# Performance work log

Hardware: AMD Instinct MI355X
Metric: run time of the kernel (lower is better)

## Reference

```python
import math
import jax, jax.numpy as jnp
import numpy as np

B = 256          # graphs per batch
N0 = 512         # nodes per graph
DEG = 16         # avg degree
E = B * N0 * DEG # total edges
F_IN = 160
H = 64
RATIO = 0.11
NUM_CLASSES = 2


def setup_inputs() -> dict:
    key = jax.random.key(0)
    ks = jax.random.split(key, 20)
    x = jax.random.normal(ks[0], (B * N0, F_IN), jnp.float32)
    # within-graph random edges: src/dst local in [0, N0) plus graph offset
    eg = E // B
    off = (jnp.arange(B, dtype=jnp.int32) * N0)[:, None]
    src = (jax.random.randint(ks[1], (B, eg), 0, N0, jnp.int32) + off).reshape(-1)
    dst = (jax.random.randint(ks[2], (B, eg), 0, N0, jnp.int32) + off).reshape(-1)
    edge_index = jnp.stack([src, dst], 0)
    s = lambda fan: 1.0 / np.sqrt(fan)
    inp = {
        'x': x,
        'edge_index': edge_index,
        'conv1_Wr': jax.random.normal(ks[3], (F_IN, H), jnp.float32) * s(F_IN),
        'conv1_Wl': jax.random.normal(ks[4], (F_IN, H), jnp.float32) * s(F_IN),
        'conv1_b': jnp.zeros((H,), jnp.float32),
        'convs_Wr': jax.random.normal(ks[5], (5, H, H), jnp.float32) * s(H),
        'convs_Wl': jax.random.normal(ks[6], (5, H, H), jnp.float32) * s(H),
        'convs_b': jnp.zeros((5, H), jnp.float32),
        'pools_Wr': jax.random.normal(ks[7], (2, H, 1), jnp.float32) * s(H),
        'pools_Wl': jax.random.normal(ks[8], (2, H, 1), jnp.float32) * s(H),
        'pools_b': jnp.zeros((2, 1), jnp.float32),
        'lin1_W': jax.random.normal(ks[9], (6 * H, H), jnp.float32) * s(6 * H),
        'lin1_b': jnp.zeros((H,), jnp.float32),
        'lin2_W': jax.random.normal(ks[10], (H, NUM_CLASSES), jnp.float32) * s(H),
        'lin2_b': jnp.zeros((NUM_CLASSES,), jnp.float32),
    }
    return inp


def _gconv(x, src, dst, emask, Wr, Wl, b, n_nodes):
    # PyG GraphConv(aggr='mean'): lin_rel(mean_{j->i} x_j) + lin_root(x)
    msg = x[src] * emask[:, None]                              # [E, F]
    agg = jax.ops.segment_sum(msg, dst, num_segments=n_nodes)  # [N, F]
    deg = jax.ops.segment_sum(emask, dst, num_segments=n_nodes)
    agg = agg / jnp.maximum(deg, 1.0)[:, None]
    return agg @ Wr + b + x @ Wl


def _sag_pool(x, src, dst, emask, Wr, Wl, b, n_per, k):
    n_nodes = B * n_per
    score = _gconv(x, src, dst, emask, Wr, Wl, b, n_nodes)[:, 0]   # [N]
    _, idx = jax.lax.top_k(score.reshape(B, n_per), k)             # [B, k]
    perm = (idx + (jnp.arange(B, dtype=jnp.int32) * n_per)[:, None]).reshape(-1)
    new_x = x[perm] * jnp.tanh(score[perm])[:, None]
    newpos = jnp.full((n_nodes,), -1, jnp.int32).at[perm].set(
        jnp.arange(B * k, dtype=jnp.int32))
    ns, nd = newpos[src], newpos[dst]
    valid = (ns >= 0) & (nd >= 0)
    new_emask = emask * valid.astype(emask.dtype)
    return new_x, jnp.where(valid, ns, 0), jnp.where(valid, nd, 0), new_emask


def _gmp(x, n_per):  # global_mean_pool with equal-size graphs
    return x.reshape(B, n_per, -1).mean(axis=1)


def reference(x, edge_index, conv1_Wr, conv1_Wl, conv1_b, convs_Wr, convs_Wl,
              convs_b, pools_Wr, pools_Wl, pools_b, lin1_W, lin1_b,
              lin2_W, lin2_b):
    src, dst = edge_index[0], edge_index[1]
    emask = jnp.ones(src.shape, x.dtype)
    n = N0
    x = jax.nn.relu(_gconv(x, src, dst, emask, conv1_Wr, conv1_Wl, conv1_b, B * n))
    xs = [_gmp(x, n)]
    for i in range(5):
        x = jax.nn.relu(_gconv(x, src, dst, emask, convs_Wr[i], convs_Wl[i],
                               convs_b[i], B * n))
        xs.append(_gmp(x, n))
        if i % 2 == 0 and i < 4:
            j = i // 2
            k = math.ceil(RATIO * n)
            x, src, dst, emask = _sag_pool(x, src, dst, emask, pools_Wr[j],
                                           pools_Wl[j], pools_b[j], n, k)
            n = k
    h = jnp.concatenate(xs, axis=-1)          # JumpingKnowledge('cat') -> [B, 6H]
    h = jax.nn.relu(h @ lin1_W + lin1_b)
    h = h @ lin2_W + lin2_b                   # dropout is identity in eval mode
    return jax.nn.log_softmax(h, axis=-1)
```

## Files before the change

kernel.cpp:

```cpp
#include <hip/hip_runtime.h>
#include <math.h>

namespace {
constexpr int NB   = 256;
constexpr int EPG  = 8192;
constexpr int ETOT = NB * EPG;
constexpr int FH   = 64;
constexpr int NN0  = NB * 512;
}

__device__ float g_feat[1][(size_t)NN0 * FH];
__device__ float g_xs[NB * 6 * FH];
__device__ int   g_esrc[2][ETOT];
__device__ int   g_edst[2][ETOT];
__device__ int   g_ecnt[2][NB];

__global__ __launch_bounds__(1024)
void front(const float* __restrict__ x,
           const int* __restrict__ esrc, const int* __restrict__ edst,
           const float* __restrict__ c1Wr, const float* __restrict__ c1Wl,
           const float* __restrict__ c1b,
           const float* __restrict__ cWr, const float* __restrict__ cWl,
           const float* __restrict__ cb,
           const float* __restrict__ pwr, const float* __restrict__ pwl,
           const float* __restrict__ pb)
{
  __shared__ float zlds[512 * 64];
  __shared__ unsigned short csrbuf[EPG];
  __shared__ __align__(16) unsigned long long u2[512];
  __shared__ float wpf[2048];
  __shared__ int scnt;
  unsigned int* hist  = reinterpret_cast<unsigned int*>(u2);
  unsigned int* start = hist + 512;
  float* __restrict__ xnew = g_feat[0];
  const int g = blockIdx.x, t = threadIdx.x;
  const int gbase = g * 512, ebase = g * EPG;
  const int lane = t & 63, w = t >> 6;
  const int ndbase = w * 32;

  auto stage_chunk = [&](int c, int p) {
    const int xb  = p ? 8192  : 0;
    const int wrO = p ? 18432 : 16384;
    const int wlO = p ? 22528 : 20480;
    #pragma unroll
    for (int i = 0; i < 2; ++i) {
      const int slot = t + i * 1024;
      const int r = slot >> 2, q = slot & 3;
      const float* gp = &x[(size_t)(gbase + r) * 160 + c * 16 + q * 4];
      float* lp = zlds + xb + (size_t)(i * 1024 + w * 64) * 4;
      __builtin_amdgcn_global_load_lds(
          (const __attribute__((address_space(1))) unsigned int*)gp,
          (__attribute__((address_space(3))) unsigned int*)lp, 16, 0, 0);
    }
    {
      const float* gp = &c1Wr[c * 1024 + t];
      float* lp = zlds + wrO + (size_t)(w * 64);
      __builtin_amdgcn_global_load_lds(
          (const __attribute__((address_space(1))) unsigned int*)gp,
          (__attribute__((address_space(3))) unsigned int*)lp, 4, 0, 0);
    }
    {
      const float* gp = &c1Wl[c * 1024 + t];
      float* lp = zlds + wlO + (size_t)(w * 64);
      __builtin_amdgcn_global_load_lds(
          (const __attribute__((address_space(1))) unsigned int*)gp,
          (__attribute__((address_space(3))) unsigned int*)lp, 4, 0, 0);
    }
  };

  if (t < 512) hist[t] = 0;
  if (t == 0) scnt = 0;
  __syncthreads();
  stage_chunk(0, 0);
  for (int e = t; e < EPG; e += 1024)
    atomicAdd(&hist[edst[ebase + e] - gbase], 1u);
  __syncthreads();
  {
    unsigned int* sA = reinterpret_cast<unsigned int*>(wpf);
    unsigned int* sB = sA + 512;
    if (t < 512) sA[t] = hist[t];
    __syncthreads();
    unsigned int *pa = sA, *pb = sB;
    for (int off = 1; off < 512; off <<= 1) {
      if (t < 512) {
        unsigned int v = pa[t];
        if (t >= off) v += pa[t - off];
        pb[t] = v;
      }
      __syncthreads();
      unsigned int* tmp = pa; pa = pb; pb = tmp;
    }
    if (t < 512) start[t] = pa[t] - hist[t];
    __syncthreads();
    unsigned int* cur = pb;
    if (t < 512) cur[t] = start[t];
    __syncthreads();
    for (int e = t; e < EPG; e += 1024) {
      const int sl = esrc[ebase + e] - gbase;
      const int dl = edst[ebase + e] - gbase;
      const unsigned int pos = atomicAdd(&cur[dl], 1u);
      csrbuf[pos] = (unsigned short)sl;
    }
  }
  __syncthreads();
  float zacc[32], xla[32];
  #pragma unroll
  for (int i = 0; i < 32; ++i) { zacc[i] = 0.f; xla[i] = 0.f; }
  #pragma unroll 1
  for (int c = 0; c < 10; ++c) {
    if (c < 9) stage_chunk(c + 1, (c + 1) & 1);
    const int p   = c & 1;
    const int xb  = p ? 8192  : 0;
    const int wrO = p ? 18432 : 16384;
    const int wlO = p ? 22528 : 20480;
    #pragma unroll 1
    for (int k4 = 0; k4 < 4; ++k4) {
      const int kb = k4 * 4;
      const float wr0 = zlds[wrO + (kb+0)*64 + lane], wr1 = zlds[wrO + (kb+1)*64 + lane],
                  wr2 = zlds[wrO + (kb+2)*64 + lane], wr3 = zlds[wrO + (kb+3)*64 + lane];
      const float wl0 = zlds[wlO + (kb+0)*64 + lane], wl1 = zlds[wlO + (kb+1)*64 + lane],
                  wl2 = zlds[wlO + (kb+2)*64 + lane], wl3 = zlds[wlO + (kb+3)*64 + lane];
      #pragma unroll
      for (int i = 0; i < 32; ++i) {
        const float4 xv = *reinterpret_cast<const float4*>(
            &zlds[xb + (ndbase + i) * 16 + kb]);
        float za = zacc[i], xa = xla[i];
        za = fmaf(xv.x, wr0, za); za = fmaf(xv.y, wr1, za);
        za = fmaf(xv.z, wr2, za); za = fmaf(xv.w, wr3, za);
        xa = fmaf(xv.x, wl0, xa); xa = fmaf(xv.y, wl1, xa);
        xa = fmaf(xv.z, wl2, xa); xa = fmaf(xv.w, wl3, xa);
        zacc[i] = za; xla[i] = xa;
      }
    }
    __syncthreads();
  }
  #pragma unroll
  for (int i = 0; i < 32; ++i)
    zlds[(ndbase + i) * 64 + lane] = zacc[i];
  __syncthreads();
  {
    const float bv = c1b[lane];
    float psum = 0.f;
    #pragma unroll 1
    for (int i = 0; i < 32; ++i) {
      const int nd = ndbase + i;
      const unsigned int s = start[nd], d = hist[nd];
      float a0 = 0.f, a1 = 0.f, a2 = 0.f, a3 = 0.f;
      unsigned int j = 0;
      for (; j + 4 <= d; j += 4) {
        const int i0 = csrbuf[s+j], i1 = csrbuf[s+j+1],
                  i2 = csrbuf[s+j+2], i3 = csrbuf[s+j+3];
        a0 += zlds[i0*64 + lane]; a1 += zlds[i1*64 + lane];
        a2 += zlds[i2*64 + lane]; a3 += zlds[i3*64 + lane];
      }
      for (; j < d; ++j) a0 += zlds[csrbuf[s+j]*64 + lane];
      float v = ((a0 + a1) + (a2 + a3)) / (float)(d > 0 ? d : 1) + xla[i] + bv;
      v = fmaxf(v, 0.f);
      zacc[i] = v;
      psum += v;
    }
    __syncthreads();
    #pragma unroll
    for (int i = 0; i < 32; ++i)
      zlds[(ndbase + i) * 64 + lane] = zacc[i];
    wpf[w * 64 + lane] = psum;
    __syncthreads();
    if (t < 64) {
      float s = 0.f;
      #pragma unroll
      for (int ww = 0; ww < 16; ++ww) s += wpf[ww*64 + t];
      g_xs[g*384 + 0 + t] = s * (1.f/512.f);
    }
  }
  #pragma unroll
  for (int i = 0; i < 32; ++i) { zacc[i] = 0.f; xla[i] = 0.f; }
  {
    float* w_r = wpf;
    float* w_l = wpf + 1024;
    #pragma unroll 1
    for (int c = 0; c < 4; ++c) {
      __syncthreads();
      w_r[t] = cWr[c * 1024 + t];
      w_l[t] = cWl[c * 1024 + t];
      __syncthreads();
      #pragma unroll 1
      for (int k4 = 0; k4 < 4; ++k4) {
        const int kb = k4 * 4;
        const float wr0 = w_r[(kb+0)*64 + lane], wr1 = w_r[(kb+1)*64 + lane],
                    wr2 = w_r[(kb+2)*64 + lane], wr3 = w_r[(kb+3)*64 + lane];
        const float wl0 = w_l[(kb+0)*64 + lane], wl1 = w_l[(kb+1)*64 + lane],
                    wl2 = w_l[(kb+2)*64 + lane], wl3 = w_l[(kb+3)*64 + lane];
        #pragma unroll
        for (int i = 0; i < 32; ++i) {
          const float4 xv = *reinterpret_cast<const float4*>(
              &zlds[(ndbase + i) * 64 + c * 16 + kb]);
          float za = zacc[i], xa = xla[i];
          za = fmaf(xv.x, wr0, za); za = fmaf(xv.y, wr1, za);
          za = fmaf(xv.z, wr2, za); za = fmaf(xv.w, wr3, za);
          xa = fmaf(xv.x, wl0, xa); xa = fmaf(xv.y, wl1, xa);
          xa = fmaf(xv.z, wl2, xa); xa = fmaf(xv.w, wl3, xa);
          zacc[i] = za; xla[i] = xa;
        }
      }
    }
  }
  __syncthreads();
  #pragma unroll
  for (int i = 0; i < 32; ++i)
    zlds[(ndbase + i) * 64 + lane] = zacc[i];
  __syncthreads();
  {
    const float bv = cb[lane];
    float psum = 0.f;
    #pragma unroll 1
    for (int i = 0; i < 32; ++i) {
      const int nd = ndbase + i;
      const unsigned int s = start[nd], d = hist[nd];
      float a0 = 0.f, a1 = 0.f, a2 = 0.f, a3 = 0.f;
      unsigned int j = 0;
      for (; j + 4 <= d; j += 4) {
        const int i0 = csrbuf[s+j], i1 = csrbuf[s+j+1],
                  i2 = csrbuf[s+j+2], i3 = csrbuf[s+j+3];
        a0 += zlds[i0*64 + lane]; a1 += zlds[i1*64 + lane];
        a2 += zlds[i2*64 + lane]; a3 += zlds[i3*64 + lane];
      }
      for (; j < d; ++j) a0 += zlds[csrbuf[s+j]*64 + lane];
      float v = ((a0 + a1) + (a2 + a3)) / (float)(d > 0 ? d : 1) + xla[i] + bv;
      v = fmaxf(v, 0.f);
      zacc[i] = v;
      psum += v;
    }
    __syncthreads();
    #pragma unroll
    for (int i = 0; i < 32; ++i)
      zlds[(ndbase + i) * 64 + lane] = zacc[i];
    wpf[w * 64 + lane] = psum;
    __syncthreads();
    if (t < 64) {
      float s = 0.f;
      #pragma unroll
      for (int ww = 0; ww < 16; ++ww) s += wpf[ww*64 + t];
      g_xs[g*384 + 64 + t] = s * (1.f/512.f);
    }
    __syncthreads();
  }
  float* zs     = wpf;
  float* swl    = wpf + 512;
  float* sscore = wpf + 1024;
  const float pwrv = pwr[lane], pwlv = pwl[lane];
  for (int nd = w; nd < 512; nd += 16) {
    const float v = zlds[nd*64 + lane];
    float a = v * pwrv, b = v * pwlv;
    #pragma unroll
    for (int off = 32; off > 0; off >>= 1) {
      a += __shfl_xor(a, off);
      b += __shfl_xor(b, off);
    }
    if (lane == 0) { zs[nd] = a; swl[nd] = b; }
  }
  __syncthreads();
  if (t < 512) {
    const unsigned int s = start[t], d = hist[t];
    float a = 0.f;
    for (unsigned int j = 0; j < d; ++j) a += zs[csrbuf[s + j]];
    sscore[t] = a / fmaxf((float)d, 1.f) + pb[0] + swl[t];
  }
  __syncthreads();
  unsigned long long* keys = u2;
  if (t < 512) {
    unsigned int u = __float_as_uint(sscore[t]);
    u = (u & 0x80000000u) ? ~u : (u | 0x80000000u);
    keys[t] = ((unsigned long long)u << 32) | (unsigned int)(~(unsigned int)t);
  }
  __syncthreads();
  for (int kk = 2; kk <= 512; kk <<= 1) {
    for (int j = kk >> 1; j > 0; j >>= 1) {
      if (t < 512) {
        const int ixj = t ^ j;
        if (ixj > t) {
          const unsigned long long a = keys[t], bk = keys[ixj];
          const bool up = ((t & kk) == 0);
          if (up ? (a < bk) : (a > bk)) { keys[t] = bk; keys[ixj] = a; }
        }
      }
      __syncthreads();
    }
  }
  short* np = reinterpret_cast<short*>(csrbuf);
  if (t < 512) np[t] = -1;
  __syncthreads();
  if (t < 57)
    np[(int)(~(unsigned int)(keys[t] & 0xffffffffull))] = (short)t;
  __syncthreads();
  for (int r = w; r < 57; r += 16) {
    const int old = (int)(~(unsigned int)(keys[r] & 0xffffffffull));
    const float sc = tanhf(sscore[old]);
    xnew[(size_t)(g*57 + r)*64 + lane] = zlds[old*64 + lane] * sc;
  }
  for (int e = t; e < EPG; e += 1024) {
    const int sl = esrc[ebase + e] - gbase;
    const int dl = edst[ebase + e] - gbase;
    const int ns = np[sl], nd2 = np[dl];
    if (ns >= 0 && nd2 >= 0) {
      const int slot = atomicAdd(&scnt, 1);
      g_esrc[0][ebase + slot] = g*57 + ns;
      g_edst[0][ebase + slot] = g*57 + nd2;
    }
  }
  __syncthreads();
  if (t == 0) g_ecnt[0][g] = scnt;
}

__device__ __forceinline__ void conv_small(
    float* X, float* Z, float* ACC, float* w_s, const float* deg,
    const float* Wr, const float* Wl, const float* bias,
    int n, const int* esrc, const int* edst, int m, int gb, int ebase,
    int xs_off, int g, int t, int lane, int w)
{
  for (int i = t; i < n*64; i += 512) { Z[i] = 0.f; ACC[i] = 0.f; }
  __syncthreads();
  for (int kc = 0; kc < 4; ++kc) {
    for (int i = t; i < 1024; i += 512) w_s[i] = Wr[kc*1024 + i];
    __syncthreads();
    for (int r = w; r < n; r += 8) {
      float zacc = 0.f;
      #pragma unroll
      for (int k = 0; k < 16; ++k)
        zacc = fmaf(X[r*64 + kc*16 + k], w_s[k*64 + lane], zacc);
      Z[r*64 + lane] += zacc;
    }
    __syncthreads();
  }
  for (int e = w; e < m; e += 8) {
    const int sl = esrc[ebase + e] - gb;
    const int dl = edst[ebase + e] - gb;
    atomicAdd(&ACC[dl*64 + lane], Z[sl*64 + lane]);
  }
  __syncthreads();
  for (int i = t; i < n*64; i += 512) {
    const int r = i >> 6, f = i & 63;
    Z[i] = ACC[i] / fmaxf(deg[r], 1.f) + bias[f];
  }
  __syncthreads();
  for (int kc = 0; kc < 4; ++kc) {
    for (int i = t; i < 1024; i += 512) w_s[i] = Wl[kc*1024 + i];
    __syncthreads();
    for (int r = w; r < n; r += 8) {
      float zacc = 0.f;
      #pragma unroll
      for (int k = 0; k < 16; ++k)
        zacc = fmaf(X[r*64 + kc*16 + k], w_s[k*64 + lane], zacc);
      Z[r*64 + lane] += zacc;
    }
    __syncthreads();
  }
  for (int i = t; i < n*64; i += 512) X[i] = fmaxf(Z[i], 0.f);
  __syncthreads();
  if (t < 64) {
    float s = 0.f;
    for (int r = 0; r < n; ++r) s += X[r*64 + t];
    g_xs[g*384 + xs_off + t] = s / (float)n;
  }
  __syncthreads();
}

__global__ __launch_bounds__(512)
void tail(const float* __restrict__ cWr, const float* __restrict__ cWl,
          const float* __restrict__ cb,
          const float* __restrict__ pWr, const float* __restrict__ pWl,
          const float* __restrict__ pb)
{
  __shared__ float X[57*64], Z[57*64], ACC[57*64];
  __shared__ float w_s[16*64];
  __shared__ float deg[64];
  __shared__ float zs[64], swl[64], sagg[64], sscore[64];
  __shared__ unsigned long long keys[64];
  __shared__ short newpos[64];
  __shared__ int scnt;
  const int g = blockIdx.x, t = threadIdx.x;
  const int lane = t & 63, w = t >> 6;
  const int ebase = g * EPG;

  for (int i = t; i < 57*64; i += 512) X[i] = g_feat[0][(size_t)(g*57)*64 + i];
  const int m0 = g_ecnt[0][g];
  if (t < 64) deg[t] = 0.f;
  __syncthreads();
  for (int e = t; e < m0; e += 512)
    atomicAdd(&deg[g_edst[0][ebase + e] - g*57], 1.f);
  __syncthreads();

  conv_small(X, Z, ACC, w_s, deg, cWr + 4096,  cWl + 4096,  cb + 64,
             57, g_esrc[0], g_edst[0], m0, g*57, ebase, 128, g, t, lane, w);
  conv_small(X, Z, ACC, w_s, deg, cWr + 8192,  cWl + 8192,  cb + 128,
             57, g_esrc[0], g_edst[0], m0, g*57, ebase, 192, g, t, lane, w);

  {
    const float pwrv = pWr[64 + lane], pwlv = pWl[64 + lane];
    for (int r = w; r < 57; r += 8) {
      float a = X[r*64 + lane] * pwrv, b = X[r*64 + lane] * pwlv;
      #pragma unroll
      for (int off = 32; off > 0; off >>= 1) {
        a += __shfl_xor(a, off);
        b += __shfl_xor(b, off);
      }
      if (lane == 0) { zs[r] = a; swl[r] = b; }
    }
    if (t < 64) sagg[t] = 0.f;
    if (t == 0) scnt = 0;
    __syncthreads();
    for (int e = t; e < m0; e += 512)
      atomicAdd(&sagg[g_edst[0][ebase + e] - g*57],
                zs[g_esrc[0][ebase + e] - g*57]);
    __syncthreads();
    if (t < 57) sscore[t] = sagg[t] / fmaxf(deg[t], 1.f) + pb[1] + swl[t];
    __syncthreads();
    if (t < 64) {
      unsigned long long key = 0ull;
      if (t < 57) {
        unsigned int u = __float_as_uint(sscore[t]);
        u = (u & 0x80000000u) ? ~u : (u | 0x80000000u);
        key = ((unsigned long long)u << 32) | (unsigned int)(~(unsigned int)t);
      }
      keys[t] = key;
    }
    __syncthreads();
    for (int kk = 2; kk <= 64; kk <<= 1) {
      for (int j = kk >> 1; j > 0; j >>= 1) {
        if (t < 64) {
          const int ixj = t ^ j;
          if (ixj > t) {
            const unsigned long long a = keys[t], bk = keys[ixj];
            const bool up = ((t & kk) == 0);
            if (up ? (a < bk) : (a > bk)) { keys[t] = bk; keys[ixj] = a; }
          }
        }
        __syncthreads();
      }
    }
    if (t < 64) newpos[t] = -1;
    __syncthreads();
    if (t < 7)
      newpos[(int)(~(unsigned int)(keys[t] & 0xffffffffull))] = (short)t;
    __syncthreads();
    for (int r = w; r < 7; r += 8) {
      const int old = (int)(~(unsigned int)(keys[r] & 0xffffffffull));
      const float sc = tanhf(sscore[old]);
      Z[r*64 + lane] = X[old*64 + lane] * sc;
    }
    for (int e = t; e < m0; e += 512) {
      const int sl = g_esrc[0][ebase + e] - g*57;
      const int dl = g_edst[0][ebase + e] - g*57;
      const int ns = newpos[sl], nd2 = newpos[dl];
      if (ns >= 0 && nd2 >= 0) {
        const int slot = atomicAdd(&scnt, 1);
        g_esrc[1][ebase + slot] = g*7 + ns;
        g_edst[1][ebase + slot] = g*7 + nd2;
      }
    }
    __syncthreads();
    for (int i = t; i < 7*64; i += 512) X[i] = Z[i];
    if (t < 64) deg[t] = 0.f;
    __syncthreads();
  }
  const int m1 = scnt;
  for (int e = t; e < m1; e += 512)
    atomicAdd(&deg[g_edst[1][ebase + e] - g*7], 1.f);
  __syncthreads();

  conv_small(X, Z, ACC, w_s, deg, cWr + 12288, cWl + 12288, cb + 192,
             7, g_esrc[1], g_edst[1], m1, g*7, ebase, 256, g, t, lane, w);
  conv_small(X, Z, ACC, w_s, deg, cWr + 16384, cWl + 16384, cb + 256,
             7, g_esrc[1], g_edst[1], m1, g*7, ebase, 320, g, t, lane, w);
}

__global__ __launch_bounds__(64)
void head(const float* __restrict__ W1, const float* __restrict__ b1,
          const float* __restrict__ W2, const float* __restrict__ b2,
          float* __restrict__ out)
{
  __shared__ float h[384], o1[64], lg[2];
  const int g = blockIdx.x, t = threadIdx.x;
  for (int i = t; i < 384; i += 64) h[i] = g_xs[g*384 + i];
  __syncthreads();
  float acc = b1[t];
  for (int j = 0; j < 384; ++j) acc = fmaf(h[j], W1[j*64 + t], acc);
  o1[t] = fmaxf(acc, 0.f);
  __syncthreads();
  if (t < 2) {
    float a2 = b2[t];
    for (int f2 = 0; f2 < 64; ++f2) a2 = fmaf(o1[f2], W2[f2*2 + t], a2);
    lg[t] = a2;
  }
  __syncthreads();
  if (t < 2) {
    const float mx = fmaxf(lg[0], lg[1]);
    const float lse = mx + logf(expf(lg[0]-mx) + expf(lg[1]-mx));
    out[g*2 + t] = lg[t] - lse;
  }
}

extern "C" void kernel_launch(void* const* d_in, const int* in_sizes, int n_in,
                              void* d_out, int out_size, void* d_ws, size_t ws_size,
                              hipStream_t stream)
{
  (void)in_sizes; (void)n_in; (void)d_ws; (void)ws_size; (void)out_size;
  const float* x    = (const float*)d_in[0];
  const int*   ei   = (const int*)d_in[1];
  const float* c1Wr = (const float*)d_in[2];
  const float* c1Wl = (const float*)d_in[3];
  const float* c1b  = (const float*)d_in[4];
  const float* cWr  = (const float*)d_in[5];
  const float* cWl  = (const float*)d_in[6];
  const float* cb   = (const float*)d_in[7];
  const float* pWr  = (const float*)d_in[8];
  const float* pWl  = (const float*)d_in[9];
  const float* pb   = (const float*)d_in[10];
  const float* l1W  = (const float*)d_in[11];
  const float* l1b  = (const float*)d_in[12];
  const float* l2W  = (const float*)d_in[13];
  const float* l2b  = (const float*)d_in[14];
  float* out = (float*)d_out;
  const int* esrc = ei;
  const int* edst = ei + ETOT;

  front<<<NB, 1024, 0, stream>>>(x, esrc, edst, c1Wr, c1Wl, c1b,
                                 cWr, cWl, cb, pWr, pWl, pb);
  tail<<<NB, 512, 0, stream>>>(cWr, cWl, cb, pWr, pWl, pb);
  head<<<NB, 64, 0, stream>>>(l1W, l1b, l2W, l2b, out);
}
```

Baseline: 334.2 us.

## Fuse front, tail and head kernels into one per-graph monolithic kernel

```diff
diff --git a/kernel.cpp b/kernel.cpp
--- a/kernel.cpp
+++ b/kernel.cpp
@@ -5,34 +5,29 @@
 constexpr int NB   = 256;
 constexpr int EPG  = 8192;
 constexpr int ETOT = NB * EPG;
-constexpr int FH   = 64;
-constexpr int NN0  = NB * 512;
 }
 
-__device__ float g_feat[1][(size_t)NN0 * FH];
-__device__ float g_xs[NB * 6 * FH];
-__device__ int   g_esrc[2][ETOT];
-__device__ int   g_edst[2][ETOT];
-__device__ int   g_ecnt[2][NB];
-
 __global__ __launch_bounds__(1024)
-void front(const float* __restrict__ x,
-           const int* __restrict__ esrc, const int* __restrict__ edst,
-           const float* __restrict__ c1Wr, const float* __restrict__ c1Wl,
-           const float* __restrict__ c1b,
-           const float* __restrict__ cWr, const float* __restrict__ cWl,
-           const float* __restrict__ cb,
-           const float* __restrict__ pwr, const float* __restrict__ pwl,
-           const float* __restrict__ pb)
+void mono(const float* __restrict__ x,
+          const int* __restrict__ esrc, const int* __restrict__ edst,
+          const float* __restrict__ c1Wr, const float* __restrict__ c1Wl,
+          const float* __restrict__ c1b,
+          const float* __restrict__ cWr, const float* __restrict__ cWl,
+          const float* __restrict__ cb,
+          const float* __restrict__ pwr, const float* __restrict__ pwl,
+          const float* __restrict__ pb,
+          const float* __restrict__ l1W, const float* __restrict__ l1b,
+          const float* __restrict__ l2W, const float* __restrict__ l2b,
+          float* __restrict__ out)
 {
   __shared__ float zlds[512 * 64];
   __shared__ unsigned short csrbuf[EPG];
   __shared__ __align__(16) unsigned long long u2[512];
   __shared__ float wpf[2048];
+  __shared__ float xsl[384];
   __shared__ int scnt;
   unsigned int* hist  = reinterpret_cast<unsigned int*>(u2);
   unsigned int* start = hist + 512;
-  float* __restrict__ xnew = g_feat[0];
   const int g = blockIdx.x, t = threadIdx.x;
   const int gbase = g * 512, ebase = g * EPG;
   const int lane = t & 63, w = t >> 6;
@@ -169,7 +164,7 @@
       float s = 0.f;
       #pragma unroll
       for (int ww = 0; ww < 16; ++ww) s += wpf[ww*64 + t];
-      g_xs[g*384 + 0 + t] = s * (1.f/512.f);
+      xsl[0 + t] = s * (1.f/512.f);
     }
   }
   #pragma unroll
@@ -240,184 +235,179 @@
       float s = 0.f;
       #pragma unroll
       for (int ww = 0; ww < 16; ++ww) s += wpf[ww*64 + t];
-      g_xs[g*384 + 64 + t] = s * (1.f/512.f);
-    }
-    __syncthreads();
-  }
-  float* zs     = wpf;
-  float* swl    = wpf + 512;
-  float* sscore = wpf + 1024;
-  const float pwrv = pwr[lane], pwlv = pwl[lane];
-  for (int nd = w; nd < 512; nd += 16) {
-    const float v = zlds[nd*64 + lane];
-    float a = v * pwrv, b = v * pwlv;
-    #pragma unroll
-    for (int off = 32; off > 0; off >>= 1) {
-      a += __shfl_xor(a, off);
-      b += __shfl_xor(b, off);
-    }
-    if (lane == 0) { zs[nd] = a; swl[nd] = b; }
-  }
-  __syncthreads();
-  if (t < 512) {
-    const unsigned int s = start[t], d = hist[t];
-    float a = 0.f;
-    for (unsigned int j = 0; j < d; ++j) a += zs[csrbuf[s + j]];
-    sscore[t] = a / fmaxf((float)d, 1.f) + pb[0] + swl[t];
-  }
-  __syncthreads();
-  unsigned long long* keys = u2;
-  if (t < 512) {
-    unsigned int u = __float_as_uint(sscore[t]);
-    u = (u & 0x80000000u) ? ~u : (u | 0x80000000u);
-    keys[t] = ((unsigned long long)u << 32) | (unsigned int)(~(unsigned int)t);
-  }
-  __syncthreads();
-  for (int kk = 2; kk <= 512; kk <<= 1) {
-    for (int j = kk >> 1; j > 0; j >>= 1) {
-      if (t < 512) {
-        const int ixj = t ^ j;
-        if (ixj > t) {
-          const unsigned long long a = keys[t], bk = keys[ixj];
-          const bool up = ((t & kk) == 0);
-          if (up ? (a < bk) : (a > bk)) { keys[t] = bk; keys[ixj] = a; }
+      xsl[64 + t] = s * (1.f/512.f);
+    }
+    __syncthreads();
+  }
+  {
+    float* zs     = wpf;
+    float* swl    = wpf + 512;
+    float* sscore = wpf + 1024;
+    const float pwrv = pwr[lane], pwlv = pwl[lane];
+    for (int nd = w; nd < 512; nd += 16) {
+      const float v = zlds[nd*64 + lane];
+      float a = v * pwrv, b = v * pwlv;
+      #pragma unroll
+      for (int off = 32; off > 0; off >>= 1) {
+        a += __shfl_xor(a, off);
+        b += __shfl_xor(b, off);
+      }
+      if (lane == 0) { zs[nd] = a; swl[nd] = b; }
+    }
+    __syncthreads();
+    if (t < 512) {
+      const unsigned int s = start[t], d = hist[t];
+      float a = 0.f;
+      for (unsigned int j = 0; j < d; ++j) a += zs[csrbuf[s + j]];
+      sscore[t] = a / fmaxf((float)d, 1.f) + pb[0] + swl[t];
+    }
+    __syncthreads();
+    unsigned long long* keys = u2;
+    if (t < 512) {
+      unsigned int u = __float_as_uint(sscore[t]);
+      u = (u & 0x80000000u) ? ~u : (u | 0x80000000u);
+      keys[t] = ((unsigned long long)u << 32) | (unsigned int)(~(unsigned int)t);
+    }
+    __syncthreads();
+    for (int kk = 2; kk <= 512; kk <<= 1) {
+      for (int j = kk >> 1; j > 0; j >>= 1) {
+        if (t < 512) {
+          const int ixj = t ^ j;
+          if (ixj > t) {
+            const unsigned long long a = keys[t], bk = keys[ixj];
+            const bool up = ((t & kk) == 0);
+            if (up ? (a < bk) : (a > bk)) { keys[t] = bk; keys[ixj] = a; }
+          }
         }
-      }
-      __syncthreads();
-    }
-  }
-  short* np = reinterpret_cast<short*>(csrbuf);
-  if (t < 512) np[t] = -1;
-  __syncthreads();
-  if (t < 57)
-    np[(int)(~(unsigned int)(keys[t] & 0xffffffffull))] = (short)t;
-  __syncthreads();
-  for (int r = w; r < 57; r += 16) {
-    const int old = (int)(~(unsigned int)(keys[r] & 0xffffffffull));
-    const float sc = tanhf(sscore[old]);
-    xnew[(size_t)(g*57 + r)*64 + lane] = zlds[old*64 + lane] * sc;
-  }
-  for (int e = t; e < EPG; e += 1024) {
-    const int sl = esrc[ebase + e] - gbase;
-    const int dl = edst[ebase + e] - gbase;
-    const int ns = np[sl], nd2 = np[dl];
-    if (ns >= 0 && nd2 >= 0) {
-      const int slot = atomicAdd(&scnt, 1);
-      g_esrc[0][ebase + slot] = g*57 + ns;
-      g_edst[0][ebase + slot] = g*57 + nd2;
-    }
-  }
-  __syncthreads();
-  if (t == 0) g_ecnt[0][g] = scnt;
-}
-
-__device__ __forceinline__ void conv_small(
-    float* X, float* Z, float* ACC, float* w_s, const float* deg,
-    const float* Wr, const float* Wl, const float* bias,
-    int n, const int* esrc, const int* edst, int m, int gb, int ebase,
-    int xs_off, int g, int t, int lane, int w)
-{
-  for (int i = t; i < n*64; i += 512) { Z[i] = 0.f; ACC[i] = 0.f; }
-  __syncthreads();
-  for (int kc = 0; kc < 4; ++kc) {
-    for (int i = t; i < 1024; i += 512) w_s[i] = Wr[kc*1024 + i];
-    __syncthreads();
-    for (int r = w; r < n; r += 8) {
-      float zacc = 0.f;
+        __syncthreads();
+      }
+    }
+    short* np = reinterpret_cast<short*>(csrbuf);
+    if (t < 512) np[t] = -1;
+    __syncthreads();
+    if (t < 57)
+      np[(int)(~(unsigned int)(keys[t] & 0xffffffffull))] = (short)t;
+    __syncthreads();
+    float xr[4];
+    int nr = 0;
+    for (int r = w * 4; r < w * 4 + 4 && r < 57; ++r) {
+      const int old = (int)(~(unsigned int)(keys[r] & 0xffffffffull));
+      xr[nr++] = zlds[old*64 + lane] * tanhf(sscore[old]);
+    }
+    if (t < 64) wpf[t] = 0.f;
+    if (t == 0) scnt = 0;
+    __syncthreads();
+    nr = 0;
+    for (int r = w * 4; r < w * 4 + 4 && r < 57; ++r)
+      zlds[r*64 + lane] = xr[nr++];
+    unsigned int* eb = reinterpret_cast<unsigned int*>(zlds + 16384);
+    for (int e = t; e < EPG; e += 1024) {
+      const int sl = esrc[ebase + e] - gbase;
+      const int dl = edst[ebase + e] - gbase;
+      const int ns = np[sl], nd2 = np[dl];
+      if (ns >= 0 && nd2 >= 0) {
+        const int slot = atomicAdd(&scnt, 1);
+        eb[slot] = (unsigned int)ns | ((unsigned int)nd2 << 16);
+        atomicAdd(&wpf[nd2], 1.f);
+      }
+    }
+    __syncthreads();
+  }
+  const int m0 = scnt;
+  float* X   = zlds;
+  float* Z   = zlds + 4096;
+  float* ACC = zlds + 8192;
+  float* deg = wpf;
+  float* w_s = wpf + 512;
+  unsigned int* eb  = reinterpret_cast<unsigned int*>(zlds + 16384);
+  unsigned int* eb1 = reinterpret_cast<unsigned int*>(zlds + 24576);
+
+  auto conv57 = [&](int n, const unsigned int* edges, int m,
+                    const float* Wr, const float* Wl, const float* bias,
+                    int xs_off) {
+    for (int i = t; i < n*64; i += 1024) { Z[i] = 0.f; ACC[i] = 0.f; }
+    __syncthreads();
+    for (int kc = 0; kc < 4; ++kc) {
+      w_s[t] = Wr[kc*1024 + t];
+      __syncthreads();
+      for (int r = w; r < n; r += 16) {
+        float za = 0.f;
+        #pragma unroll
+        for (int k = 0; k < 16; ++k)
+          za = fmaf(X[r*64 + kc*16 + k], w_s[k*64 + lane], za);
+        Z[r*64 + lane] += za;
+      }
+      __syncthreads();
+    }
+    for (int e = w; e < m; e += 16) {
+      const unsigned int pr = edges[e];
+      const int sl = pr & 0xffff, dl = pr >> 16;
+      atomicAdd(&ACC[dl*64 + lane], Z[sl*64 + lane]);
+    }
+    __syncthreads();
+    for (int i = t; i < n*64; i += 1024) {
+      const int r = i >> 6, f = i & 63;
+      Z[i] = ACC[i] / fmaxf(deg[r], 1.f) + bias[f];
+    }
+    __syncthreads();
+    for (int kc = 0; kc < 4; ++kc) {
+      w_s[t] = Wl[kc*1024 + t];
+      __syncthreads();
+      for (int r = w; r < n; r += 16) {
+        float za = 0.f;
+        #pragma unroll
+        for (int k = 0; k < 16; ++k)
+          za = fmaf(X[r*64 + kc*16 + k], w_s[k*64 + lane], za);
+        Z[r*64 + lane] += za;
+      }
+      __syncthreads();
+    }
+    for (int i = t; i < n*64; i += 1024) X[i] = fmaxf(Z[i], 0.f);
+    __syncthreads();
+    float psum = 0.f;
+    for (int r = w; r < n; r += 16) psum += X[r*64 + lane];
+    Z[w*64 + lane] = psum;
+    __syncthreads();
+    if (t < 64) {
+      float s = 0.f;
       #pragma unroll
-      for (int k = 0; k < 16; ++k)
-        zacc = fmaf(X[r*64 + kc*16 + k], w_s[k*64 + lane], zacc);
-      Z[r*64 + lane] += zacc;
-    }
-    __syncthreads();
-  }
-  for (int e = w; e < m; e += 8) {
-    const int sl = esrc[ebase + e] - gb;
-    const int dl = edst[ebase + e] - gb;
-    atomicAdd(&ACC[dl*64 + lane], Z[sl*64 + lane]);
-  }
-  __syncthreads();
-  for (int i = t; i < n*64; i += 512) {
-    const int r = i >> 6, f = i & 63;
-    Z[i] = ACC[i] / fmaxf(deg[r], 1.f) + bias[f];
-  }
-  __syncthreads();
-  for (int kc = 0; kc < 4; ++kc) {
-    for (int i = t; i < 1024; i += 512) w_s[i] = Wl[kc*1024 + i];
-    __syncthreads();
-    for (int r = w; r < n; r += 8) {
-      float zacc = 0.f;
-      #pragma unroll
-      for (int k = 0; k < 16; ++k)
-        zacc = fmaf(X[r*64 + kc*16 + k], w_s[k*64 + lane], zacc);
-      Z[r*64 + lane] += zacc;
-    }
-    __syncthreads();
-  }
-  for (int i = t; i < n*64; i += 512) X[i] = fmaxf(Z[i], 0.f);
-  __syncthreads();
-  if (t < 64) {
-    float s = 0.f;
-    for (int r = 0; r < n; ++r) s += X[r*64 + t];
-    g_xs[g*384 + xs_off + t] = s / (float)n;
-  }
-  __syncthreads();
-}
-
-__global__ __launch_bounds__(512)
-void tail(const float* __restrict__ cWr, const float* __restrict__ cWl,
-          const float* __restrict__ cb,
-          const float* __restrict__ pWr, const float* __restrict__ pWl,
-          const float* __restrict__ pb)
-{
-  __shared__ float X[57*64], Z[57*64], ACC[57*64];
-  __shared__ float w_s[16*64];
-  __shared__ float deg[64];
-  __shared__ float zs[64], swl[64], sagg[64], sscore[64];
-  __shared__ unsigned long long keys[64];
-  __shared__ short newpos[64];
-  __shared__ int scnt;
-  const int g = blockIdx.x, t = threadIdx.x;
-  const int lane = t & 63, w = t >> 6;
-  const int ebase = g * EPG;
-
-  for (int i = t; i < 57*64; i += 512) X[i] = g_feat[0][(size_t)(g*57)*64 + i];
-  const int m0 = g_ecnt[0][g];
-  if (t < 64) deg[t] = 0.f;
-  __syncthreads();
-  for (int e = t; e < m0; e += 512)
-    atomicAdd(&deg[g_edst[0][ebase + e] - g*57], 1.f);
-  __syncthreads();
-
-  conv_small(X, Z, ACC, w_s, deg, cWr + 4096,  cWl + 4096,  cb + 64,
-             57, g_esrc[0], g_edst[0], m0, g*57, ebase, 128, g, t, lane, w);
-  conv_small(X, Z, ACC, w_s, deg, cWr + 8192,  cWl + 8192,  cb + 128,
-             57, g_esrc[0], g_edst[0], m0, g*57, ebase, 192, g, t, lane, w);
+      for (int ww = 0; ww < 16; ++ww) s += Z[ww*64 + t];
+      xsl[xs_off + t] = s / (float)n;
+    }
+    __syncthreads();
+  };
+
+  conv57(57, eb, m0, cWr + 4096, cWl + 4096, cb + 64, 128);
+  conv57(57, eb, m0, cWr + 8192, cWl + 8192, cb + 128, 192);
 
   {
-    const float pwrv = pWr[64 + lane], pwlv = pWl[64 + lane];
-    for (int r = w; r < 57; r += 8) {
+    float* zs1 = wpf + 1536;
+    float* sw1 = wpf + 1600;
+    float* ss1 = wpf + 1664;
+    const float pwrv = pwr[64 + lane], pwlv = pwl[64 + lane];
+    for (int r = w; r < 57; r += 16) {
       float a = X[r*64 + lane] * pwrv, b = X[r*64 + lane] * pwlv;
       #pragma unroll
       for (int off = 32; off > 0; off >>= 1) {
         a += __shfl_xor(a, off);
         b += __shfl_xor(b, off);
       }
-      if (lane == 0) { zs[r] = a; swl[r] = b; }
-    }
-    if (t < 64) sagg[t] = 0.f;
-    if (t == 0) scnt = 0;
-    __syncthreads();
-    for (int e = t; e < m0; e += 512)
-      atomicAdd(&sagg[g_edst[0][ebase + e] - g*57],
-                zs[g_esrc[0][ebase + e] - g*57]);
-    __syncthreads();
-    if (t < 57) sscore[t] = sagg[t] / fmaxf(deg[t], 1.f) + pb[1] + swl[t];
-    __syncthreads();
+      if (lane == 0) { zs1[r] = a; sw1[r] = b; }
+    }
+    if (t >= 64 && t < 128) ACC[t - 64] = 0.f;
+    __syncthreads();
+    for (int e = t; e < m0; e += 1024) {
+      const unsigned int pr = eb[e];
+      atomicAdd(&ACC[pr >> 16], zs1[pr & 0xffff]);
+    }
+    __syncthreads();
+    if (t < 57) ss1[t] = ACC[t] / fmaxf(deg[t], 1.f) + pb[1] + sw1[t];
+    __syncthreads();
+    unsigned long long* keys = u2;
     if (t < 64) {
       unsigned long long key = 0ull;
       if (t < 57) {
-        unsigned int u = __float_as_uint(sscore[t]);
+        unsigned int u = __float_as_uint(ss1[t]);
         u = (u & 0x80000000u) ? ~u : (u | 0x80000000u);
         key = ((unsigned long long)u << 32) | (unsigned int)(~(unsigned int)t);
       }
@@ -437,65 +427,54 @@
         __syncthreads();
       }
     }
-    if (t < 64) newpos[t] = -1;
+    short* np1 = reinterpret_cast<short*>(csrbuf);
+    if (t < 64) np1[t] = -1;
     __syncthreads();
     if (t < 7)
-      newpos[(int)(~(unsigned int)(keys[t] & 0xffffffffull))] = (short)t;
-    __syncthreads();
-    for (int r = w; r < 7; r += 8) {
-      const int old = (int)(~(unsigned int)(keys[r] & 0xffffffffull));
-      const float sc = tanhf(sscore[old]);
-      Z[r*64 + lane] = X[old*64 + lane] * sc;
-    }
-    for (int e = t; e < m0; e += 512) {
-      const int sl = g_esrc[0][ebase + e] - g*57;
-      const int dl = g_edst[0][ebase + e] - g*57;
-      const int ns = newpos[sl], nd2 = newpos[dl];
+      np1[(int)(~(unsigned int)(keys[t] & 0xffffffffull))] = (short)t;
+    __syncthreads();
+    float xv7 = 0.f;
+    int old7 = -1;
+    if (w < 7 && w * 4 == w * 4) {
+      old7 = (int)(~(unsigned int)(keys[w] & 0xffffffffull));
+      xv7 = X[old7*64 + lane] * tanhf(ss1[old7]);
+    }
+    if (t < 64) deg[t] = 0.f;
+    if (t == 0) scnt = 0;
+    __syncthreads();
+    if (w < 7) X[w*64 + lane] = xv7;
+    for (int e = t; e < m0; e += 1024) {
+      const unsigned int pr = eb[e];
+      const int ns = np1[pr & 0xffff], nd2 = np1[pr >> 16];
       if (ns >= 0 && nd2 >= 0) {
         const int slot = atomicAdd(&scnt, 1);
-        g_esrc[1][ebase + slot] = g*7 + ns;
-        g_edst[1][ebase + slot] = g*7 + nd2;
-      }
-    }
-    __syncthreads();
-    for (int i = t; i < 7*64; i += 512) X[i] = Z[i];
-    if (t < 64) deg[t] = 0.f;
+        eb1[slot] = (unsigned int)ns | ((unsigned int)nd2 << 16);
+        atomicAdd(&deg[nd2], 1.f);
+      }
+    }
     __syncthreads();
   }
   const int m1 = scnt;
-  for (int e = t; e < m1; e += 512)
-    atomicAdd(&deg[g_edst[1][ebase + e] - g*7], 1.f);
-  __syncthreads();
-
-  conv_small(X, Z, ACC, w_s, deg, cWr + 12288, cWl + 12288, cb + 192,
-             7, g_esrc[1], g_edst[1], m1, g*7, ebase, 256, g, t, lane, w);
-  conv_small(X, Z, ACC, w_s, deg, cWr + 16384, cWl + 16384, cb + 256,
-             7, g_esrc[1], g_edst[1], m1, g*7, ebase, 320, g, t, lane, w);
-}
-
-__global__ __launch_bounds__(64)
-void head(const float* __restrict__ W1, const float* __restrict__ b1,
-          const float* __restrict__ W2, const float* __restrict__ b2,
-          float* __restrict__ out)
-{
-  __shared__ float h[384], o1[64], lg[2];
-  const int g = blockIdx.x, t = threadIdx.x;
-  for (int i = t; i < 384; i += 64) h[i] = g_xs[g*384 + i];
-  __syncthreads();
-  float acc = b1[t];
-  for (int j = 0; j < 384; ++j) acc = fmaf(h[j], W1[j*64 + t], acc);
-  o1[t] = fmaxf(acc, 0.f);
+
+  conv57(7, eb1, m1, cWr + 12288, cWl + 12288, cb + 192, 256);
+  conv57(7, eb1, m1, cWr + 16384, cWl + 16384, cb + 256, 320);
+
+  if (t < 64) {
+    float acc = l1b[t];
+    for (int j = 0; j < 384; ++j) acc = fmaf(xsl[j], l1W[j*64 + t], acc);
+    wpf[t] = fmaxf(acc, 0.f);
+  }
   __syncthreads();
   if (t < 2) {
-    float a2 = b2[t];
-    for (int f2 = 0; f2 < 64; ++f2) a2 = fmaf(o1[f2], W2[f2*2 + t], a2);
-    lg[t] = a2;
+    float a2 = l2b[t];
+    for (int f2 = 0; f2 < 64; ++f2) a2 = fmaf(wpf[f2], l2W[f2*2 + t], a2);
+    wpf[64 + t] = a2;
   }
   __syncthreads();
   if (t < 2) {
-    const float mx = fmaxf(lg[0], lg[1]);
-    const float lse = mx + logf(expf(lg[0]-mx) + expf(lg[1]-mx));
-    out[g*2 + t] = lg[t] - lse;
+    const float mx = fmaxf(wpf[64], wpf[65]);
+    const float lse = mx + logf(expf(wpf[64]-mx) + expf(wpf[65]-mx));
+    out[g*2 + t] = wpf[64 + t] - lse;
   }
 }
 
@@ -523,8 +502,7 @@
   const int* esrc = ei;
   const int* edst = ei + ETOT;
 
-  front<<<NB, 1024, 0, stream>>>(x, esrc, edst, c1Wr, c1Wl, c1b,
-                                 cWr, cWl, cb, pWr, pWl, pb);
-  tail<<<NB, 512, 0, stream>>>(cWr, cWl, cb, pWr, pWl, pb);
-  head<<<NB, 64, 0, stream>>>(l1W, l1b, l2W, l2b, out);
+  mono<<<NB, 1024, 0, stream>>>(x, esrc, edst, c1Wr, c1Wl, c1b,
+                                cWr, cWl, cb, pWr, pWl, pb,
+                                l1W, l1b, l2W, l2b, out);
 }
```

Measured after the change: 320.4 us. -4.1%, faster.
